# Optimization experiments

Measured on AMD Instinct MI355X. Metric: run time of the kernel, lower is better.

## Reference

```python
import math
from itertools import combinations
import jax, jax.numpy as jnp
import numpy as np

SEQ_LEN = 8
D_IN = 2048
D_OUT = 1152
TSS = 3          # temporal_set_size
WAY = 5
SHOT = 5
N_SUPPORT = WAY * SHOT
N_Q = 100
PE_SCALE = 0.1
LN_EPS = 1e-5

TUPLES = np.array(list(combinations(range(SEQ_LEN), TSS)), dtype=np.int32)  # [56, 3]
T_LEN = TUPLES.shape[0]  # 56


def _positional_encoding(seq_len, d):
    pos = np.arange(seq_len, dtype=np.float32)[:, None]
    div = np.exp(np.arange(0, d, 2, dtype=np.float32) * -(math.log(10000.0) / d))
    pe = np.zeros((seq_len, d), dtype=np.float32)
    pe[:, 0::2] = np.sin(pos * div) * PE_SCALE
    pe[:, 1::2] = np.cos(pos * div) * PE_SCALE
    return jnp.asarray(pe)


def _layernorm(x, g, b):
    mu = jnp.mean(x, axis=-1, keepdims=True)
    var = jnp.mean((x - mu) ** 2, axis=-1, keepdims=True)
    return (x - mu) * jax.lax.rsqrt(var + LN_EPS) * g + b


def setup_inputs() -> dict:
    key = jax.random.key(0)
    ks = jax.random.split(key, 6)
    support_set = jax.random.normal(ks[0], (N_SUPPORT, SEQ_LEN, D_IN), dtype=jnp.float32)
    queries = jax.random.normal(ks[1], (N_Q, SEQ_LEN, D_IN), dtype=jnp.float32)
    # sorted episode layout: class c occupies rows [c*SHOT, (c+1)*SHOT)
    support_labels = jnp.repeat(jnp.arange(WAY, dtype=jnp.int64), SHOT)
    d_flat = TSS * D_IN  # 6144
    k_w = jax.random.normal(ks[2], (d_flat, D_OUT), dtype=jnp.float32) * 0.02
    k_b = jnp.zeros((D_OUT,), dtype=jnp.float32)
    v_w = jax.random.normal(ks[3], (d_flat, D_OUT), dtype=jnp.float32) * 0.02
    v_b = jnp.zeros((D_OUT,), dtype=jnp.float32)
    ln_g = jnp.ones((D_OUT,), dtype=jnp.float32)
    ln_b = jnp.zeros((D_OUT,), dtype=jnp.float32)
    return {"support_set": support_set, "queries": queries,
            "support_labels": support_labels,
            "k_w": k_w, "k_b": k_b, "v_w": v_w, "v_b": v_b,
            "ln_g": ln_g, "ln_b": ln_b}


def reference(support_set, queries, support_labels, k_w, k_b, v_w, v_b, ln_g, ln_b):
    pe = _positional_encoding(SEQ_LEN, D_IN)  # dropout is identity in eval mode
    s = support_set + pe
    q = queries + pe

    def tuplify(x):  # [N, S, D] -> [N, T_LEN, TSS*D]
        return x[:, TUPLES, :].reshape(x.shape[0], T_LEN, TSS * D_IN)

    s_t = tuplify(s)
    q_t = tuplify(q)

    sk = _layernorm(s_t @ k_w + k_b, ln_g, ln_b)  # [25, 56, 1152]
    qk = _layernorm(q_t @ k_w + k_b, ln_g, ln_b)  # [100, 56, 1152]
    sv = s_t @ v_w + v_b                           # [25, 56, 1152]
    qv = q_t @ v_w + v_b                           # [100, 56, 1152]

    scale = 1.0 / math.sqrt(D_OUT)
    dists = []
    align = None
    for c in range(WAY):  # fixed small class loop; class rows are a static slice
        class_k = sk[c * SHOT:(c + 1) * SHOT]  # [SHOT, 56, 1152]
        class_v = sv[c * SHOT:(c + 1) * SHOT]
        # scores: [Q, T, K, T] == torch permute(0,2,1,3) of [Q, K, T, T]
        scores = jnp.einsum('qtd,ksd->qtks', qk, class_k) * scale
        flat = scores.reshape(N_Q, T_LEN, SHOT * T_LEN)
        sm = jax.nn.softmax(flat, axis=-1)
        sm = sm.reshape(N_Q, T_LEN, SHOT, T_LEN).transpose(0, 2, 1, 3)  # [Q, K, T, T]
        align = sm.sum(axis=1)  # [Q, T, T]
        proto = jnp.einsum('qkts,ksd->qtd', sm, class_v)  # [Q, 56, 1152]
        diff = qv - proto
        dists.append(-jnp.sum(diff * diff, axis=(-2, -1)) / T_LEN)  # [Q]
    logits = jnp.stack(dists, axis=1)  # [Q, WAY]
    return logits, align
```

## Files before the change

### kernel.cpp

```cpp
#include <hip/hip_runtime.h>
#include <hip/hip_bf16.h>
#include <math.h>

#define SEQ_LEN 8
#define D_IN 2048
#define D_OUT 1152
#define WAY 5
#define SHOT 5
#define N_SUPPORT 25
#define N_Q 100
#define N_SEQ 125
#define N_ROWS 1000
#define T_LEN 56
#define KS_LEN 280
#define KS_PAD 288
#define NCOLS 6912
#define MQT 5600
#define DPC 18

typedef __attribute__((ext_vector_type(4))) float f32x4;
typedef __attribute__((ext_vector_type(8))) short bf16x8;

__constant__ int TUP[T_LEN][3] = {
  {0,1,2},{0,1,3},{0,1,4},{0,1,5},{0,1,6},{0,1,7},{0,2,3},{0,2,4},{0,2,5},{0,2,6},
  {0,2,7},{0,3,4},{0,3,5},{0,3,6},{0,3,7},{0,4,5},{0,4,6},{0,4,7},{0,5,6},{0,5,7},
  {0,6,7},{1,2,3},{1,2,4},{1,2,5},{1,2,6},{1,2,7},{1,3,4},{1,3,5},{1,3,6},{1,3,7},
  {1,4,5},{1,4,6},{1,4,7},{1,5,6},{1,5,7},{1,6,7},{2,3,4},{2,3,5},{2,3,6},{2,3,7},
  {2,4,5},{2,4,6},{2,4,7},{2,5,6},{2,5,7},{2,6,7},{3,4,5},{3,4,6},{3,4,7},{3,5,6},
  {3,5,7},{3,6,7},{4,5,6},{4,5,7},{4,6,7},{5,6,7}
};

__device__ __forceinline__ ushort f2bf(float f) {
  union { float f; unsigned u; } v; v.f = f;
  unsigned r = v.u + 0x7FFFu + ((v.u >> 16) & 1u);
  return (ushort)(r >> 16);
}
__device__ __forceinline__ float bf2f(ushort u) {
  union { unsigned u; float f; } v; v.u = ((unsigned)u) << 16;
  return v.f;
}
__device__ __forceinline__ void gload16(const void* g, const void* l) {
  __builtin_amdgcn_global_load_lds(
      (const __attribute__((address_space(1))) unsigned int*)g,
      (__attribute__((address_space(3))) unsigned int*)l, 16, 0, 0);
}
template<int N> __device__ __forceinline__ void vmw() {
  asm volatile("s_waitcnt vmcnt(%0)" :: "n"(N) : "memory");
}

__global__ __launch_bounds__(256) void pe_add(const float* __restrict__ sup,
                                              const float* __restrict__ que,
                                              ushort* __restrict__ X) {
  int idx = blockIdx.x * 256 + threadIdx.x;
  if (idx >= N_ROWS * D_IN) return;
  int d = idx & (D_IN - 1);
  int r = idx >> 11;
  int i = r & 7;
  int h2 = d & ~1;
  float freq = expf((float)h2 * (-9.210340371976184f / (float)D_IN));
  float ang = (float)i * freq;
  float pe = ((d & 1) ? cosf(ang) : sinf(ang)) * 0.1f;
  float src = (r < N_SUPPORT * SEQ_LEN) ? sup[idx] : que[idx - N_SUPPORT * SEQ_LEN * D_IN];
  X[idx] = f2bf(src + pe);
}

__global__ __launch_bounds__(256) void wtrans(const float* __restrict__ kw,
                                              const float* __restrict__ vw,
                                              ushort* __restrict__ WT) {
  __shared__ float tile[64][65];
  int bx = blockIdx.x;
  int by = blockIdx.y;
  int b = bx / 18;
  int n0 = (bx % 18) * 64;
  int k0 = by * 64;
  const float* src = ((b & 1) ? vw : kw) + (size_t)(b >> 1) * D_IN * D_OUT;
  int tid = threadIdx.x;
#pragma unroll
  for (int it = 0; it < 4; ++it) {
    int lin4 = it * 256 + tid;
    int kk = lin4 >> 4;
    int n4 = (lin4 & 15) * 4;
    float4 v = *(const float4*)(src + (size_t)(k0 + kk) * D_OUT + n0 + n4);
    tile[kk][n4 + 0] = v.x; tile[kk][n4 + 1] = v.y;
    tile[kk][n4 + 2] = v.z; tile[kk][n4 + 3] = v.w;
  }
  __syncthreads();
#pragma unroll
  for (int it = 0; it < 4; ++it) {
    int lin = it * 1024 + tid * 4;
    int nn = lin >> 6, kk = lin & 63;
    ushort4 o;
    o.x = f2bf(tile[kk + 0][nn]); o.y = f2bf(tile[kk + 1][nn]);
    o.z = f2bf(tile[kk + 2][nn]); o.w = f2bf(tile[kk + 3][nn]);
    *(ushort4*)&WT[((size_t)(b * D_OUT + n0 + nn)) * D_IN + k0 + kk] = o;
  }
}

template<int EPI, int NT>
__global__ __launch_bounds__(256) void gemm_bt(
    const ushort* __restrict__ A, const ushort* __restrict__ BT,
    float* __restrict__ C,
    const ushort* __restrict__ QV, float* __restrict__ DP,
    int M, int N, int K, int lda, int ldb, int ldc, float alpha,
    long batchA, long batchB, long batchC) {
  constexpr int JF = NT / 32;
  constexpr int NCH = 8 + NT / 16;
  __shared__ ushort As[2][128][32];
  __shared__ ushort Bs[2][NT][32];
  int z = blockIdx.z;
  A  += (size_t)z * batchA;
  BT += (size_t)z * batchB;
  if constexpr (EPI < 2) C  += (size_t)z * batchC;
  else                   DP += (size_t)z * batchC;

  int tid = threadIdx.x;
  int wid = tid >> 6, lane = tid & 63;
  int l16 = lane & 15, lk = lane >> 4;
  int wr = wid >> 1, wc = wid & 1;
  int row0 = blockIdx.x * 128, col0 = blockIdx.y * NT;
  int lrow = lane >> 2;
  int lcol = ((lane & 3) ^ ((lane >> 3) & 3)) * 8;
  int rslot = (lk ^ ((l16 >> 1) & 3)) * 8;

  auto stage = [&](int buf, int t) {
    int k0 = t * 32;
    for (int c = wid; c < NCH; c += 4) {
      if (c < 8) {
        int grow = row0 + c * 16 + lrow;
        grow = grow < M ? grow : M - 1;
        gload16(A + (size_t)grow * lda + k0 + lcol, &As[buf][c * 16][0]);
      } else {
        int gcol = col0 + (c - 8) * 16 + lrow;
        gcol = gcol < N ? gcol : N - 1;
        gload16(BT + (size_t)gcol * ldb + k0 + lcol, &Bs[buf][(c - 8) * 16][0]);
      }
    }
  };

  f32x4 acc[4][JF] = {};
  int nk = K / 32;
  stage(0, 0);
  for (int t = 0; t < nk; ++t) {
    int cur = t & 1;
    if (t + 1 < nk) {
      stage(cur ^ 1, t + 1);
      if constexpr ((NCH & 3) == 0) {
        vmw<NCH / 4>();
      } else {
        if (wid < (NCH & 3)) vmw<NCH / 4 + 1>(); else vmw<NCH / 4>();
      }
    } else {
      vmw<0>();
    }
    __builtin_amdgcn_s_barrier();
    __builtin_amdgcn_sched_barrier(0);
    bf16x8 af[4], bv[JF];
#pragma unroll
    for (int m = 0; m < 4; ++m)
      af[m] = *(const bf16x8*)&As[cur][wr * 64 + m * 16 + l16][rslot];
#pragma unroll
    for (int j = 0; j < JF; ++j)
      bv[j] = *(const bf16x8*)&Bs[cur][wc * (NT / 2) + j * 16 + l16][rslot];
#pragma unroll
    for (int m = 0; m < 4; ++m)
#pragma unroll
      for (int j = 0; j < JF; ++j)
        acc[m][j] = __builtin_amdgcn_mfma_f32_16x16x32_bf16(af[m], bv[j], acc[m][j], 0, 0, 0);
    __builtin_amdgcn_sched_barrier(0);
    __builtin_amdgcn_s_barrier();
  }

  if constexpr (EPI < 2) {
#pragma unroll
    for (int m = 0; m < 4; ++m)
#pragma unroll
      for (int j = 0; j < JF; ++j) {
        int col = col0 + wc * (NT / 2) + j * 16 + l16;
#pragma unroll
        for (int r = 0; r < 4; ++r) {
          int row = row0 + wr * 64 + m * 16 + lk * 4 + r;
          if (row < M && col < N)
            C[(size_t)row * ldc + col] = (EPI == 1) ? acc[m][j][r] * alpha : acc[m][j][r];
        }
      }
  } else {
    float sq[4][4] = {};
#pragma unroll
    for (int m = 0; m < 4; ++m)
#pragma unroll
      for (int j = 0; j < JF; ++j) {
        int col = col0 + wc * (NT / 2) + j * 16 + l16;
#pragma unroll
        for (int r = 0; r < 4; ++r) {
          int row = row0 + wr * 64 + m * 16 + lk * 4 + r;
          if (row < M) {
            float qvv = bf2f(QV[(size_t)row * D_OUT + col]);
            float d = qvv - acc[m][j][r];
            sq[m][r] += d * d;
          }
        }
      }
#pragma unroll
    for (int m = 0; m < 4; ++m)
#pragma unroll
      for (int r = 0; r < 4; ++r) {
        sq[m][r] += __shfl_xor(sq[m][r], 1);
        sq[m][r] += __shfl_xor(sq[m][r], 2);
        sq[m][r] += __shfl_xor(sq[m][r], 4);
        sq[m][r] += __shfl_xor(sq[m][r], 8);
      }
    if (l16 == 0) {
#pragma unroll
      for (int m = 0; m < 4; ++m)
#pragma unroll
        for (int r = 0; r < 4; ++r) {
          int row = row0 + wr * 64 + m * 16 + lk * 4 + r;
          if (row < M) DP[(size_t)row * DPC + blockIdx.y * 2 + wc] = sq[m][r];
        }
    }
  }
}

__global__ __launch_bounds__(256) void combine_ln(const float* __restrict__ G,
                                                  const float* __restrict__ kb,
                                                  const float* __restrict__ vb,
                                                  const float* __restrict__ lng,
                                                  const float* __restrict__ lnb,
                                                  ushort* __restrict__ skbf,
                                                  ushort* __restrict__ qkbf,
                                                  ushort* __restrict__ sv,
                                                  ushort* __restrict__ qvbf) {
  int t = blockIdx.x;
  int n = blockIdx.y;
  const float* g0 = G + (size_t)(n * 8 + TUP[t][0]) * NCOLS;
  const float* g1 = G + (size_t)(n * 8 + TUP[t][1]) * NCOLS + 2 * D_OUT;
  const float* g2 = G + (size_t)(n * 8 + TUP[t][2]) * NCOLS + 4 * D_OUT;
  __shared__ float kbuf[D_OUT];
  __shared__ float red1[256], red2[256];
  int tid = threadIdx.x;
  bool isq = (n >= N_SUPPORT);
  int c = n / SHOT, s = n % SHOT;
  ushort* vout = isq ? qvbf + ((size_t)(n - N_SUPPORT) * T_LEN + t) * D_OUT
                     : sv + ((size_t)c * KS_PAD + s * T_LEN + t) * D_OUT;
  float s1 = 0.f, s2 = 0.f;
  for (int d4 = tid; d4 < D_OUT / 4; d4 += 256) {
    int d = d4 * 4;
    float4 a = *(const float4*)(g0 + d);
    float4 b = *(const float4*)(g0 + D_OUT + d);
    float4 c1 = *(const float4*)(g1 + d);
    float4 c2 = *(const float4*)(g1 + D_OUT + d);
    float4 e1 = *(const float4*)(g2 + d);
    float4 e2 = *(const float4*)(g2 + D_OUT + d);
    float4 kb4 = *(const float4*)(kb + d);
    float4 vb4 = *(const float4*)(vb + d);
    float kx = a.x + c1.x + e1.x + kb4.x, ky = a.y + c1.y + e1.y + kb4.y;
    float kz = a.z + c1.z + e1.z + kb4.z, kw = a.w + c1.w + e1.w + kb4.w;
    float vx = b.x + c2.x + e2.x + vb4.x, vy = b.y + c2.y + e2.y + vb4.y;
    float vz = b.z + c2.z + e2.z + vb4.z, vw = b.w + c2.w + e2.w + vb4.w;
    *(float4*)(kbuf + d) = make_float4(kx, ky, kz, kw);
    ushort4 vv; vv.x = f2bf(vx); vv.y = f2bf(vy); vv.z = f2bf(vz); vv.w = f2bf(vw);
    *(ushort4*)(vout + d) = vv;
    s1 += kx + ky + kz + kw;
    s2 += kx * kx + ky * ky + kz * kz + kw * kw;
  }
  red1[tid] = s1; red2[tid] = s2;
  __syncthreads();
  for (int sft = 128; sft > 0; sft >>= 1) {
    if (tid < sft) { red1[tid] += red1[tid + sft]; red2[tid] += red2[tid + sft]; }
    __syncthreads();
  }
  float mu = red1[0] * (1.0f / D_OUT);
  float var = red2[0] * (1.0f / D_OUT) - mu * mu;
  float rs = rsqrtf(var + 1e-5f);
  ushort* kout = isq ? qkbf + ((size_t)(n - N_SUPPORT) * T_LEN + t) * D_OUT
                     : skbf + ((size_t)c * KS_PAD + s * T_LEN + t) * D_OUT;
  for (int d4 = tid; d4 < D_OUT / 4; d4 += 256) {
    int d = d4 * 4;
    float4 kv = *(const float4*)(kbuf + d);
    float4 g4 = *(const float4*)(lng + d);
    float4 b4 = *(const float4*)(lnb + d);
    ushort4 o;
    o.x = f2bf((kv.x - mu) * rs * g4.x + b4.x);
    o.y = f2bf((kv.y - mu) * rs * g4.y + b4.y);
    o.z = f2bf((kv.z - mu) * rs * g4.z + b4.z);
    o.w = f2bf((kv.w - mu) * rs * g4.w + b4.w);
    *(ushort4*)(kout + d) = o;
  }
}

__global__ __launch_bounds__(256) void svtrans(const ushort* __restrict__ sv,
                                               ushort* __restrict__ svT) {
  __shared__ ushort tile[32][65];
  int c = blockIdx.z;
  int d0 = blockIdx.x * 64;
  int k0 = blockIdx.y * 32;
  const ushort* src = sv + (size_t)c * KS_PAD * D_OUT;
  ushort* dst = svT + (size_t)c * D_OUT * KS_PAD;
  int tid = threadIdx.x;
#pragma unroll
  for (int it = 0; it < 8; ++it) {
    int lin = it * 256 + tid;
    int ks = k0 + (lin >> 6), d = d0 + (lin & 63);
    tile[lin >> 6][lin & 63] = (ks < KS_LEN) ? src[(size_t)ks * D_OUT + d] : (ushort)0;
  }
  __syncthreads();
#pragma unroll
  for (int it = 0; it < 8; ++it) {
    int lin = it * 256 + tid;
    int d = lin >> 5, ks = lin & 31;
    dst[(size_t)(d0 + d) * KS_PAD + k0 + ks] = tile[ks][d];
  }
}

__global__ __launch_bounds__(256) void softmax_align(const float* __restrict__ S,
                                                     ushort* __restrict__ sm,
                                                     float* __restrict__ align_out) {
  __shared__ float pl[4][KS_LEN];
  int wid = threadIdx.x >> 6, lane = threadIdx.x & 63;
  int row = blockIdx.x * 4 + wid;
  const float* src = S + (size_t)row * KS_PAD;
  float v[5];
  float mx = -1e30f;
#pragma unroll
  for (int j = 0; j < 5; ++j) {
    int ks = lane + j * 64;
    v[j] = (ks < KS_LEN) ? src[ks] : -1e30f;
    mx = fmaxf(mx, v[j]);
  }
#pragma unroll
  for (int m = 32; m > 0; m >>= 1) mx = fmaxf(mx, __shfl_xor(mx, m));
  float sum = 0.f;
  float p[5];
#pragma unroll
  for (int j = 0; j < 5; ++j) {
    int ks = lane + j * 64;
    p[j] = (ks < KS_LEN) ? expf(v[j] - mx) : 0.f;
    sum += p[j];
  }
#pragma unroll
  for (int m = 32; m > 0; m >>= 1) sum += __shfl_xor(sum, m);
  float inv = 1.0f / sum;
  ushort* dst = sm + (size_t)row * KS_PAD;
#pragma unroll
  for (int j = 0; j < 5; ++j) {
    int ks = lane + j * 64;
    if (ks < KS_PAD) dst[ks] = f2bf((ks < KS_LEN) ? p[j] * inv : 0.f);
  }
  int c = row / MQT;
  if (c == WAY - 1) {
#pragma unroll
    for (int j = 0; j < 5; ++j) {
      int ks = lane + j * 64;
      if (ks < KS_LEN) pl[wid][ks] = p[j] * inv;
    }
    __syncthreads();
    if (lane < T_LEN) {
      float a = 0.f;
#pragma unroll
      for (int k = 0; k < SHOT; ++k) a += pl[wid][k * T_LEN + lane];
      int qt = row - (WAY - 1) * MQT;
      align_out[(size_t)(qt / T_LEN) * (T_LEN * T_LEN) + (qt % T_LEN) * T_LEN + lane] = a;
    }
  }
}

__global__ __launch_bounds__(256) void logits_k(const float* __restrict__ DP,
                                                float* __restrict__ out) {
  __shared__ float red[256];
  int q = blockIdx.x / WAY, c = blockIdx.x % WAY;
  const float* base = DP + ((size_t)c * MQT + q * T_LEN) * DPC;
  int tid = threadIdx.x;
  float s = 0.f;
  for (int i = tid; i < T_LEN * DPC; i += 256) s += base[i];
  red[tid] = s;
  __syncthreads();
  for (int sft = 128; sft > 0; sft >>= 1) {
    if (tid < sft) red[tid] += red[tid + sft];
    __syncthreads();
  }
  if (tid == 0) out[blockIdx.x] = -red[0] * (1.0f / T_LEN);
}

extern "C" void kernel_launch(void* const* d_in, const int* in_sizes, int n_in,
                              void* d_out, int out_size, void* d_ws, size_t ws_size,
                              hipStream_t stream) {
  const float* sup  = (const float*)d_in[0];
  const float* que  = (const float*)d_in[1];
  const float* k_w  = (const float*)d_in[3];
  const float* k_b  = (const float*)d_in[4];
  const float* v_w  = (const float*)d_in[5];
  const float* v_b  = (const float*)d_in[6];
  const float* ln_g = (const float*)d_in[7];
  const float* ln_b = (const float*)d_in[8];
  float* out = (float*)d_out;

  char* w = (char*)d_ws;
  ushort* Xbf  = (ushort*)(w + 0);
  ushort* WT   = (ushort*)(w + 4096000);
  float*  G    = (float*)(w + 32407552);
  ushort* sv   = (ushort*)(w + 0);
  float*  S    = (float*)(w + 0);
  ushort* smbf = (ushort*)(w + 32407552);
  float*  DP   = (float*)(w + 0);
  ushort* qkbf = (ushort*)(w + 60055552);
  ushort* skbf = (ushort*)(w + 72957952);
  ushort* svT  = (ushort*)(w + 76275712);
  ushort* qvbf = (ushort*)(w + 79593472);

  const float scale = 0.02946278254943948f;

  pe_add<<<dim3(8000), 256, 0, stream>>>(sup, que, Xbf);
  wtrans<<<dim3(108, 32), 256, 0, stream>>>(k_w, v_w, WT);
  gemm_bt<0, 64><<<dim3(8, 108, 1), 256, 0, stream>>>(
      Xbf, WT, G, nullptr, nullptr,
      N_ROWS, NCOLS, D_IN, D_IN, D_IN, NCOLS, 1.0f, 0, 0, 0);
  combine_ln<<<dim3(T_LEN, N_SEQ), 256, 0, stream>>>(
      G, k_b, v_b, ln_g, ln_b, skbf, qkbf, sv, qvbf);
  svtrans<<<dim3(18, 9, WAY), 256, 0, stream>>>(sv, svT);
  gemm_bt<1, 96><<<dim3(44, 3, WAY), 256, 0, stream>>>(
      qkbf, skbf, S, nullptr, nullptr,
      MQT, KS_PAD, D_OUT, D_OUT, D_OUT, KS_PAD, scale,
      0, (long)KS_PAD * D_OUT, (long)MQT * KS_PAD);
  softmax_align<<<dim3(7000), 256, 0, stream>>>(S, smbf, out + N_Q * WAY);
  gemm_bt<2, 128><<<dim3(44, 9, WAY), 256, 0, stream>>>(
      smbf, svT, nullptr, qvbf, DP,
      MQT, D_OUT, KS_PAD, KS_PAD, KS_PAD, 0, 1.0f,
      (long)MQT * KS_PAD, (long)D_OUT * KS_PAD, (long)MQT * DPC);
  logits_k<<<dim3(N_Q * WAY), 256, 0, stream>>>(DP, out);
}
```

Before: 233.6 us.

## Add dedicated PV-distance kernel with resident B tile; warp-per-row combine_ln

Replaces the generic double-buffered GEMM used for the softmax-times-values distance step with a dedicated kernel. That kernel loads the whole 128x288 svT tile into LDS once and streams A fragments straight from global memory across the nine K steps, with each wave covering 32 rows by 128 columns. This removes the per-K-step staging and barriers, and it halves the number of partial-distance columns. Separately, combine_ln now uses one wavefront per (sequence, tuple) row and reduces with shuffles instead of LDS tree reductions and block syncs. The trade-off is that A reads now go uncoalesced from global memory, and the larger LDS footprint may lower occupancy.

```diff
diff --git a/kernel.cpp b/kernel.cpp
--- a/kernel.cpp
+++ b/kernel.cpp
@@ -16,7 +16,7 @@
 #define KS_PAD 288
 #define NCOLS 6912
 #define MQT 5600
-#define DPC 18
+#define DPC 9
 
 typedef __attribute__((ext_vector_type(4))) float f32x4;
 typedef __attribute__((ext_vector_type(8))) short bf16x8;
@@ -100,7 +100,6 @@
 __global__ __launch_bounds__(256) void gemm_bt(
     const ushort* __restrict__ A, const ushort* __restrict__ BT,
     float* __restrict__ C,
-    const ushort* __restrict__ QV, float* __restrict__ DP,
     int M, int N, int K, int lda, int ldb, int ldc, float alpha,
     long batchA, long batchB, long batchC) {
   constexpr int JF = NT / 32;
@@ -110,8 +109,7 @@
   int z = blockIdx.z;
   A  += (size_t)z * batchA;
   BT += (size_t)z * batchB;
-  if constexpr (EPI < 2) C  += (size_t)z * batchC;
-  else                   DP += (size_t)z * batchC;
+  C  += (size_t)z * batchC;
 
   int tid = threadIdx.x;
   int wid = tid >> 6, lane = tid & 63;
@@ -170,54 +168,95 @@
     __builtin_amdgcn_s_barrier();
   }
 
-  if constexpr (EPI < 2) {
-#pragma unroll
-    for (int m = 0; m < 4; ++m)
-#pragma unroll
-      for (int j = 0; j < JF; ++j) {
-        int col = col0 + wc * (NT / 2) + j * 16 + l16;
-#pragma unroll
-        for (int r = 0; r < 4; ++r) {
-          int row = row0 + wr * 64 + m * 16 + lk * 4 + r;
-          if (row < M && col < N)
-            C[(size_t)row * ldc + col] = (EPI == 1) ? acc[m][j][r] * alpha : acc[m][j][r];
-        }
+#pragma unroll
+  for (int m = 0; m < 4; ++m)
+#pragma unroll
+    for (int j = 0; j < JF; ++j) {
+      int col = col0 + wc * (NT / 2) + j * 16 + l16;
+#pragma unroll
+      for (int r = 0; r < 4; ++r) {
+        int row = row0 + wr * 64 + m * 16 + lk * 4 + r;
+        if (row < M && col < N)
+          C[(size_t)row * ldc + col] = (EPI == 1) ? acc[m][j][r] * alpha : acc[m][j][r];
       }
-  } else {
-    float sq[4][4] = {};
-#pragma unroll
-    for (int m = 0; m < 4; ++m)
-#pragma unroll
-      for (int j = 0; j < JF; ++j) {
-        int col = col0 + wc * (NT / 2) + j * 16 + l16;
-#pragma unroll
-        for (int r = 0; r < 4; ++r) {
-          int row = row0 + wr * 64 + m * 16 + lk * 4 + r;
-          if (row < M) {
-            float qvv = bf2f(QV[(size_t)row * D_OUT + col]);
-            float d = qvv - acc[m][j][r];
-            sq[m][r] += d * d;
-          }
-        }
+    }
+}
+
+__global__ __launch_bounds__(256) void pv_dist(const ushort* __restrict__ SM,
+                                               const ushort* __restrict__ SVT,
+                                               const ushort* __restrict__ QV,
+                                               float* __restrict__ DP) {
+  __shared__ ushort Bs[128][296];
+  int tid = threadIdx.x, wid = tid >> 6, lane = tid & 63;
+  int l16 = lane & 15, lk = lane >> 4;
+  int row0 = blockIdx.x * 128, col0 = blockIdx.y * 128, c = blockIdx.z;
+  const ushort* sm = SM + (size_t)c * MQT * KS_PAD;
+  const ushort* bt = SVT + ((size_t)c * D_OUT + col0) * KS_PAD;
+  {
+    int r = tid >> 1, h = tid & 1;
+    const ushort* srcr = bt + (size_t)r * KS_PAD + h * 144;
+#pragma unroll
+    for (int i = 0; i < 18; ++i) {
+      uint4 v = *(const uint4*)(srcr + i * 8);
+      *(uint4*)&Bs[r][h * 144 + i * 8] = v;
+    }
+  }
+  __syncthreads();
+
+  int ra0 = row0 + wid * 32 + l16;      if (ra0 > MQT - 1) ra0 = MQT - 1;
+  int ra1 = row0 + wid * 32 + 16 + l16; if (ra1 > MQT - 1) ra1 = MQT - 1;
+  const ushort* a0 = sm + (size_t)ra0 * KS_PAD + lk * 8;
+  const ushort* a1 = sm + (size_t)ra1 * KS_PAD + lk * 8;
+
+  f32x4 acc[2][8] = {};
+#pragma unroll
+  for (int ks = 0; ks < 9; ++ks) {
+    bf16x8 af0 = *(const bf16x8*)(a0 + ks * 32);
+    bf16x8 af1 = *(const bf16x8*)(a1 + ks * 32);
+    bf16x8 bv[8];
+#pragma unroll
+    for (int j = 0; j < 8; ++j)
+      bv[j] = *(const bf16x8*)&Bs[j * 16 + l16][ks * 32 + lk * 8];
+#pragma unroll
+    for (int j = 0; j < 8; ++j) {
+      acc[0][j] = __builtin_amdgcn_mfma_f32_16x16x32_bf16(af0, bv[j], acc[0][j], 0, 0, 0);
+      acc[1][j] = __builtin_amdgcn_mfma_f32_16x16x32_bf16(af1, bv[j], acc[1][j], 0, 0, 0);
+    }
+  }
+
+  float sq[2][4] = {};
+#pragma unroll
+  for (int m = 0; m < 2; ++m)
+#pragma unroll
+    for (int r = 0; r < 4; ++r) {
+      int row = row0 + wid * 32 + m * 16 + lk * 4 + r;
+      int rowc = row < MQT ? row : MQT - 1;
+      const ushort* qvr = QV + (size_t)rowc * D_OUT + col0;
+#pragma unroll
+      for (int j = 0; j < 8; ++j) {
+        float qvv = bf2f(qvr[j * 16 + l16]);
+        float d = qvv - acc[m][j][r];
+        sq[m][r] += d * d;
       }
-#pragma unroll
-    for (int m = 0; m < 4; ++m)
+    }
+#pragma unroll
+  for (int m = 0; m < 2; ++m)
+#pragma unroll
+    for (int r = 0; r < 4; ++r) {
+      sq[m][r] += __shfl_xor(sq[m][r], 1);
+      sq[m][r] += __shfl_xor(sq[m][r], 2);
+      sq[m][r] += __shfl_xor(sq[m][r], 4);
+      sq[m][r] += __shfl_xor(sq[m][r], 8);
+    }
+  if (l16 == 0) {
+    float* dp = DP + (size_t)c * MQT * DPC;
+#pragma unroll
+    for (int m = 0; m < 2; ++m)
 #pragma unroll
       for (int r = 0; r < 4; ++r) {
-        sq[m][r] += __shfl_xor(sq[m][r], 1);
-        sq[m][r] += __shfl_xor(sq[m][r], 2);
-        sq[m][r] += __shfl_xor(sq[m][r], 4);
-        sq[m][r] += __shfl_xor(sq[m][r], 8);
+        int row = row0 + wid * 32 + m * 16 + lk * 4 + r;
+        if (row < MQT) dp[(size_t)row * DPC + blockIdx.y] = sq[m][r];
       }
-    if (l16 == 0) {
-#pragma unroll
-      for (int m = 0; m < 4; ++m)
-#pragma unroll
-        for (int r = 0; r < 4; ++r) {
-          int row = row0 + wr * 64 + m * 16 + lk * 4 + r;
-          if (row < M) DP[(size_t)row * DPC + blockIdx.y * 2 + wc] = sq[m][r];
-        }
-    }
   }
 }
 
@@ -230,61 +269,57 @@
                                                   ushort* __restrict__ qkbf,
                                                   ushort* __restrict__ sv,
                                                   ushort* __restrict__ qvbf) {
-  int t = blockIdx.x;
-  int n = blockIdx.y;
+  int gw = blockIdx.x * 4 + (threadIdx.x >> 6);
+  int lane = threadIdx.x & 63;
+  int t = gw % T_LEN, n = gw / T_LEN;
   const float* g0 = G + (size_t)(n * 8 + TUP[t][0]) * NCOLS;
   const float* g1 = G + (size_t)(n * 8 + TUP[t][1]) * NCOLS + 2 * D_OUT;
   const float* g2 = G + (size_t)(n * 8 + TUP[t][2]) * NCOLS + 4 * D_OUT;
-  __shared__ float kbuf[D_OUT];
-  __shared__ float red1[256], red2[256];
-  int tid = threadIdx.x;
   bool isq = (n >= N_SUPPORT);
   int c = n / SHOT, s = n % SHOT;
   ushort* vout = isq ? qvbf + ((size_t)(n - N_SUPPORT) * T_LEN + t) * D_OUT
                      : sv + ((size_t)c * KS_PAD + s * T_LEN + t) * D_OUT;
-  float s1 = 0.f, s2 = 0.f;
-  for (int d4 = tid; d4 < D_OUT / 4; d4 += 256) {
-    int d = d4 * 4;
-    float4 a = *(const float4*)(g0 + d);
-    float4 b = *(const float4*)(g0 + D_OUT + d);
-    float4 c1 = *(const float4*)(g1 + d);
-    float4 c2 = *(const float4*)(g1 + D_OUT + d);
-    float4 e1 = *(const float4*)(g2 + d);
-    float4 e2 = *(const float4*)(g2 + D_OUT + d);
-    float4 kb4 = *(const float4*)(kb + d);
-    float4 vb4 = *(const float4*)(vb + d);
-    float kx = a.x + c1.x + e1.x + kb4.x, ky = a.y + c1.y + e1.y + kb4.y;
-    float kz = a.z + c1.z + e1.z + kb4.z, kw = a.w + c1.w + e1.w + kb4.w;
-    float vx = b.x + c2.x + e2.x + vb4.x, vy = b.y + c2.y + e2.y + vb4.y;
-    float vz = b.z + c2.z + e2.z + vb4.z, vw = b.w + c2.w + e2.w + vb4.w;
-    *(float4*)(kbuf + d) = make_float4(kx, ky, kz, kw);
-    ushort4 vv; vv.x = f2bf(vx); vv.y = f2bf(vy); vv.z = f2bf(vz); vv.w = f2bf(vw);
-    *(ushort4*)(vout + d) = vv;
-    s1 += kx + ky + kz + kw;
-    s2 += kx * kx + ky * ky + kz * kz + kw * kw;
-  }
-  red1[tid] = s1; red2[tid] = s2;
-  __syncthreads();
-  for (int sft = 128; sft > 0; sft >>= 1) {
-    if (tid < sft) { red1[tid] += red1[tid + sft]; red2[tid] += red2[tid + sft]; }
-    __syncthreads();
-  }
-  float mu = red1[0] * (1.0f / D_OUT);
-  float var = red2[0] * (1.0f / D_OUT) - mu * mu;
-  float rs = rsqrtf(var + 1e-5f);
   ushort* kout = isq ? qkbf + ((size_t)(n - N_SUPPORT) * T_LEN + t) * D_OUT
                      : skbf + ((size_t)c * KS_PAD + s * T_LEN + t) * D_OUT;
-  for (int d4 = tid; d4 < D_OUT / 4; d4 += 256) {
-    int d = d4 * 4;
-    float4 kv = *(const float4*)(kbuf + d);
-    float4 g4 = *(const float4*)(lng + d);
-    float4 b4 = *(const float4*)(lnb + d);
-    ushort4 o;
-    o.x = f2bf((kv.x - mu) * rs * g4.x + b4.x);
-    o.y = f2bf((kv.y - mu) * rs * g4.y + b4.y);
-    o.z = f2bf((kv.z - mu) * rs * g4.z + b4.z);
-    o.w = f2bf((kv.w - mu) * rs * g4.w + b4.w);
-    *(ushort4*)(kout + d) = o;
+  float kvx[9], kvy[9], s1 = 0.f, s2 = 0.f;
+#pragma unroll
+  for (int i = 0; i < 9; ++i) {
+    int d = i * 128 + lane * 2;
+    float2 a = *(const float2*)(g0 + d);
+    float2 b = *(const float2*)(g0 + D_OUT + d);
+    float2 c1 = *(const float2*)(g1 + d);
+    float2 c2 = *(const float2*)(g1 + D_OUT + d);
+    float2 e1 = *(const float2*)(g2 + d);
+    float2 e2 = *(const float2*)(g2 + D_OUT + d);
+    float2 kb2 = *(const float2*)(kb + d);
+    float2 vb2 = *(const float2*)(vb + d);
+    float kx = a.x + c1.x + e1.x + kb2.x;
+    float ky = a.y + c1.y + e1.y + kb2.y;
+    float vx = b.x + c2.x + e2.x + vb2.x;
+    float vy = b.y + c2.y + e2.y + vb2.y;
+    kvx[i] = kx; kvy[i] = ky;
+    ushort2 vv; vv.x = f2bf(vx); vv.y = f2bf(vy);
+    *(ushort2*)(vout + d) = vv;
+    s1 += kx + ky;
+    s2 += kx * kx + ky * ky;
+  }
+#pragma unroll
+  for (int m = 32; m > 0; m >>= 1) {
+    s1 += __shfl_xor(s1, m);
+    s2 += __shfl_xor(s2, m);
+  }
+  float mu = s1 * (1.0f / D_OUT);
+  float var = s2 * (1.0f / D_OUT) - mu * mu;
+  float rs = rsqrtf(var + 1e-5f);
+#pragma unroll
+  for (int i = 0; i < 9; ++i) {
+    int d = i * 128 + lane * 2;
+    float2 g2v = *(const float2*)(lng + d);
+    float2 b2v = *(const float2*)(lnb + d);
+    ushort2 o;
+    o.x = f2bf((kvx[i] - mu) * rs * g2v.x + b2v.x);
+    o.y = f2bf((kvy[i] - mu) * rs * g2v.y + b2v.y);
+    *(ushort2*)(kout + d) = o;
   }
 }
 
@@ -412,19 +447,16 @@
   pe_add<<<dim3(8000), 256, 0, stream>>>(sup, que, Xbf);
   wtrans<<<dim3(108, 32), 256, 0, stream>>>(k_w, v_w, WT);
   gemm_bt<0, 64><<<dim3(8, 108, 1), 256, 0, stream>>>(
-      Xbf, WT, G, nullptr, nullptr,
+      Xbf, WT, G,
       N_ROWS, NCOLS, D_IN, D_IN, D_IN, NCOLS, 1.0f, 0, 0, 0);
-  combine_ln<<<dim3(T_LEN, N_SEQ), 256, 0, stream>>>(
+  combine_ln<<<dim3(1750), 256, 0, stream>>>(
       G, k_b, v_b, ln_g, ln_b, skbf, qkbf, sv, qvbf);
   svtrans<<<dim3(18, 9, WAY), 256, 0, stream>>>(sv, svT);
   gemm_bt<1, 96><<<dim3(44, 3, WAY), 256, 0, stream>>>(
-      qkbf, skbf, S, nullptr, nullptr,
+      qkbf, skbf, S,
       MQT, KS_PAD, D_OUT, D_OUT, D_OUT, KS_PAD, scale,
       0, (long)KS_PAD * D_OUT, (long)MQT * KS_PAD);
   softmax_align<<<dim3(7000), 256, 0, stream>>>(S, smbf, out + N_Q * WAY);
-  gemm_bt<2, 128><<<dim3(44, 9, WAY), 256, 0, stream>>>(
-      smbf, svT, nullptr, qvbf, DP,
-      MQT, D_OUT, KS_PAD, KS_PAD, KS_PAD, 0, 1.0f,
-      (long)MQT * KS_PAD, (long)D_OUT * KS_PAD, (long)MQT * DPC);
+  pv_dist<<<dim3(44, 9, WAY), 256, 0, stream>>>(smbf, svT, qvbf, DP);
   logits_k<<<dim3(N_Q * WAY), 256, 0, stream>>>(DP, out);
 }
```

Result: faster. 195.9 us (-16.1%).
